# Performance work log

Measured on AMD Instinct MI355X. Metric: run time of the kernel, lower is better.

## Reference

```python
import jax, jax.numpy as jnp
import numpy as np

K = 16          # patch_size
P2 = 256        # patch_size**2
D_PD = 512      # learned base dictionary atoms (D_out_lam_pd)
D_LAM = 112     # adaptive atoms from sdict, = 8*14 (D_out_lam)
DD = D_PD + D_LAM  # 624
T = 5
INDICE = 112
MIN_V, MAX_V = 0.0, 1.0


def _idx(H, W, k, stride):
    oh = (H - k) // stride + 1
    ow = (W - k) // stride + 1
    r = jnp.arange(k)[:, None] + stride * jnp.arange(oh)[None, :]  # [k, oh]
    c = jnp.arange(k)[:, None] + stride * jnp.arange(ow)[None, :]  # [k, ow]
    return r[:, None, :, None], c[None, :, None, :], oh, ow


def _unfold(x, k, stride):
    # torch.nn.Unfold: [N, C*k*k, L] with (C, kh, kw) channel order, row-major L
    N, C, H, W = x.shape
    r, c, oh, ow = _idx(H, W, k, stride)
    return x[:, :, r, c].reshape(N, C * k * k, oh * ow)


def _fold(p, H, W, k):
    # torch.nn.functional.fold (col2im) with stride 1, overlap-add
    N, ckk, L = p.shape
    r, c, oh, ow = _idx(H, W, k, 1)
    C = ckk // (k * k)
    out = jnp.zeros((N, C, H, W), p.dtype)
    return out.at[:, :, r, c].add(p.reshape(N, C, k, k, oh, ow))


def _mlp(x, ws):
    # Linear + clamp(min=0) chain, no relu after last layer (dropout = eval identity)
    for w, b in ws[:-1]:
        x = jnp.maximum(x @ w + b, 0.0)
    w, b = ws[-1]
    return x @ w + b


def _cbam(x, w1, w2, conv_w):
    # standard CBAM: channel attention (shared MLP on avg+max pool) then 7x7 spatial attention
    def mlp(v):
        return jnp.maximum(v @ w1, 0.0) @ w2
    ca = jax.nn.sigmoid(mlp(x.mean(axis=(2, 3))) + mlp(x.max(axis=(2, 3))))
    x = x * ca[:, :, None, None]
    s = jnp.stack([x.mean(axis=1), x.max(axis=1)], axis=1)  # [N,2,h,w]
    sa = jax.lax.conv_general_dilated(s, conv_w, (1, 1), [(3, 3), (3, 3)],
                                      dimension_numbers=('NCHW', 'OIHW', 'NCHW'))
    return x * jax.nn.sigmoid(sa)


def _soft(x, l):
    return jnp.sign(x) * jnp.maximum(jnp.abs(x) - l, 0.0)


def _stage(img, Dict, c, sd_ws, ca1, ca2, saw, lam_ws, pd_ws, w_ws):
    N, C, H, W = img.shape
    uf = _unfold(img, K, 1).transpose(0, 2, 1)     # [N, L, 256]
    uf1 = _unfold(img, K, 8).transpose(0, 2, 1)    # [N, L1, 256]
    step = uf1.shape[1] // INDICE                  # static under jit
    ext = uf1[:, ::step, :][:, :INDICE, :]         # [N, 112, 256]
    sd = _mlp(ext, sd_ws)                          # linears1..4
    sd = sd / jnp.maximum(jnp.linalg.norm(sd, axis=-1, keepdims=True), 1e-12)
    sd = _cbam(sd.transpose(0, 2, 1).reshape(N, P2, 8, 14), ca1, ca2, saw)
    sd = sd.reshape(N, P2, INDICE)                 # [N, 256, 112]
    Dcat = jnp.concatenate([jnp.broadcast_to(Dict, (N,) + Dict.shape), sd], axis=-1)  # [N,256,624]
    # thresholds: l = cat(lpd, ls)
    thr = jnp.concatenate([_mlp(uf, pd_ws) / c, _mlp(uf, lam_ws) / c], axis=-1)  # [N,L,624]
    y = uf @ Dcat                                  # [N, L, 624]
    # S = (I - D^T D / c)^T; D^T D is symmetric so the transpose is a no-op
    S = jnp.eye(DD, dtype=img.dtype) - (Dcat.transpose(0, 2, 1) @ Dcat) / c
    z = _soft(y, thr)
    for _ in range(T):  # LISTA unrolled iterations (T static)
        z = _soft(z @ S + y / c, thr)
    Wg = jax.nn.sigmoid(_mlp(uf, w_ws))            # [N, L, 256]
    x_pred = jnp.clip(z @ Dcat.transpose(0, 2, 1), MIN_V, MAX_V) * Wg
    num = _fold(x_pred.transpose(0, 2, 1), H, W, K)
    den = _fold(Wg.transpose(0, 2, 1), H, W, K)    # fold of W * ones
    return num / den


def _forward(x, Dict, c, s1w, s1b, s2w, s2b, s3w, s3b, s4w, s4b, caw1, caw2, saw,
             a1w, a1b, a2w, a2b, a3w, a3b, p1w, p1b, p2w, p2b, p3w, p3b,
             b1w, b1b, b2w, b2b, b3w, b3b, q1w, q1b, q2w, q2b, q3w, q3b,
             w1w, w1b, w2w, w2b, w3w, w3b):
    sd_ws = [(s1w, s1b), (s2w, s2b), (s3w, s3b), (s4w, s4b)]
    w_ws = [(w1w, w1b), (w2w, w2b), (w3w, w3b)]
    res = _stage(x, Dict, c, sd_ws, caw1, caw2, saw,
                 [(a1w, a1b), (a2w, a2b), (a3w, a3b)],
                 [(p1w, p1b), (p2w, p2b), (p3w, p3b)], w_ws)
    res = _stage(res, Dict, c, sd_ws, caw1, caw2, saw,
                 [(b1w, b1b), (b2w, b2b), (b3w, b3b)],
                 [(q1w, q1b), (q2w, q2b), (q3w, q3b)], w_ws)
    return res


def setup_inputs() -> dict:
    key = jax.random.key(0)
    ks = iter(jax.random.split(key, 40))
    d = {}
    d['x'] = jax.random.uniform(next(ks), (2, 1, 128, 128), jnp.float32)
    Dm = jax.random.normal(next(ks), (P2, D_PD), jnp.float32)
    d['Dict'] = Dm / jnp.linalg.norm(Dm, axis=0, keepdims=True)  # unit-norm atoms
    d['c'] = jnp.asarray(10.0, jnp.float32)  # c > ||D^T D||_2
    dims = {'s1': (256, 512), 's2': (512, 1024), 's3': (1024, 512), 's4': (512, 256),
            'a1': (256, 1024), 'a2': (1024, 512), 'a3': (512, 112),
            'p1': (256, 1024), 'p2': (1024, 512), 'p3': (512, 512),
            'b1': (256, 1024), 'b2': (1024, 512), 'b3': (512, 112),
            'q1': (256, 1024), 'q2': (1024, 512), 'q3': (512, 512),
            'w1': (256, 1024), 'w2': (1024, 512), 'w3': (512, 256)}
    for name, (i, o) in dims.items():
        d[name + 'w'] = jax.random.normal(next(ks), (i, o), jnp.float32) / np.float32(np.sqrt(i))
        d[name + 'b'] = jnp.zeros((o,), jnp.float32)
    d['caw1'] = jax.random.normal(next(ks), (256, 512), jnp.float32) / np.float32(16.0)
    d['caw2'] = jax.random.normal(next(ks), (512, 256), jnp.float32) / np.float32(np.sqrt(512))
    d['saw'] = jax.random.normal(next(ks), (1, 2, 7, 7), jnp.float32) * np.float32(0.1)
    return d


def reference(x, Dict, c, s1w, s1b, s2w, s2b, s3w, s3b, s4w, s4b, caw1, caw2, saw,
              a1w, a1b, a2w, a2b, a3w, a3b, p1w, p1b, p2w, p2b, p3w, p3b,
              b1w, b1b, b2w, b2b, b3w, b3b, q1w, q1b, q2w, q2b, q3w, q3b,
              w1w, w1b, w2w, w2b, w3w, w3b):
    return _forward(x, Dict, c, s1w, s1b, s2w, s2b, s3w, s3b, s4w, s4b, caw1, caw2, saw,
                    a1w, a1b, a2w, a2b, a3w, a3b, p1w, p1b, p2w, p2b, p3w, p3b,
                    b1w, b1b, b2w, b2b, b3w, b3b, q1w, q1b, q2w, q2b, q3w, q3b,
                    w1w, w1b, w2w, w2b, w3w, w3b)
```

## Files before the change

### kernel.cpp

```cpp
#include <hip/hip_runtime.h>
#include <hip/hip_bf16.h>
#include <math.h>

#define L_LOC 12769
#define NB 2
#define NLR (NB * L_LOC)
#define NW 19

typedef short short8v __attribute__((ext_vector_type(8)));
typedef float f32x4 __attribute__((ext_vector_type(4)));
typedef __hip_bfloat16 bf16;

__device__ __forceinline__ float softf(float x, float l) {
  float a = fmaxf(fabsf(x) - l, 0.0f);
  return x > 0.0f ? a : (x < 0.0f ? -a : 0.0f);
}
__device__ __forceinline__ float sigf(float x) { return 1.0f / (1.0f + expf(-x)); }
__device__ __forceinline__ void split2(float v, bf16& h, bf16& l) {
  h = __float2bfloat16(v);
  l = __float2bfloat16(v - __bfloat162float(h));
}

enum { ME_RELU = 0, ME_SCALE = 1, ME_SIG = 2, ME_Y = 3, ME_SOFT = 4, ME_XP = 5,
       ME_SMAT = 6, ME_LIN = 7 };

template <int EPI, int TERMS, int WLO>
__global__ __launch_bounds__(256) void mgemm_k(
    const bf16* __restrict__ A, int lda, size_t aOff,
    const bf16* __restrict__ B0, const bf16* __restrict__ B1, int ldb, size_t bOff,
    void* __restrict__ Cv, int ldc, size_t cOff,
    bf16* __restrict__ Zp,
    const float* __restrict__ bias,
    const void* __restrict__ E1, const void* __restrict__ E2, int lde,
    const float* __restrict__ cptr, int bRow, int Rc, int r0, int N, int K)
{
  const int NPA = (TERMS >= 3) ? 2 : 1;
  const int NPB = (TERMS >= 2) ? 2 : 1;
  __shared__ char As[(TERMS >= 3) ? 2 : 1][8192];
  __shared__ char Bs[(TERMS >= 2) ? 2 : 1][8192];
  const int t = threadIdx.x;
  const int lane = t & 63, wv = t >> 6;
  const int wr = wv >> 1, wc = wv & 1;
  const int m0 = blockIdx.y * 128, n0 = blockIdx.x * 128;
  const int nb = (m0 >= bRow) ? 1 : 0;
  const bf16* __restrict__ Bt = nb ? B1 : B0;
  const int row16 = lane & 15, kg = lane >> 4;
  const int grow = t >> 2;
  const int gcol = (t & 3) * 8;
  f32x4 acc[4][4];
#pragma unroll
  for (int i = 0; i < 4; ++i)
#pragma unroll
    for (int j = 0; j < 4; ++j) { acc[i][j][0] = 0.f; acc[i][j][1] = 0.f; acc[i][j][2] = 0.f; acc[i][j][3] = 0.f; }

  for (int k0 = 0; k0 < K; k0 += 32) {
#pragma unroll
    for (int h = 0; h < NPA; ++h)
#pragma unroll
      for (int i = 0; i < 2; ++i) {
        const bf16* ga = A + h * aOff + (size_t)(m0 + i * 64 + grow) * lda + k0 + gcol;
        __builtin_amdgcn_global_load_lds(
            (const __attribute__((address_space(1))) void*)ga,
            (__attribute__((address_space(3))) void*)(As[h] + i * 4096 + wv * 1024), 16, 0, 0);
      }
#pragma unroll
    for (int h = 0; h < NPB; ++h)
#pragma unroll
      for (int i = 0; i < 2; ++i) {
        const bf16* gb = Bt + h * bOff + (size_t)(n0 + i * 64 + grow) * ldb + k0 + gcol;
        __builtin_amdgcn_global_load_lds(
            (const __attribute__((address_space(1))) void*)gb,
            (__attribute__((address_space(3))) void*)(Bs[h] + i * 4096 + wv * 1024), 16, 0, 0);
      }
    __syncthreads();
    short8v ah[4], al[4], bh[4], bl[4];
#pragma unroll
    for (int mi = 0; mi < 4; ++mi) {
      int o = (wr * 64 + mi * 16 + row16) * 64 + kg * 16;
      ah[mi] = *(const short8v*)(As[0] + o);
      if (TERMS >= 3) al[mi] = *(const short8v*)(As[NPA - 1] + o);
    }
#pragma unroll
    for (int ni = 0; ni < 4; ++ni) {
      int o = (wc * 64 + ni * 16 + row16) * 64 + kg * 16;
      bh[ni] = *(const short8v*)(Bs[0] + o);
      if (TERMS >= 2) bl[ni] = *(const short8v*)(Bs[NPB - 1] + o);
    }
#pragma unroll
    for (int mi = 0; mi < 4; ++mi)
#pragma unroll
      for (int ni = 0; ni < 4; ++ni) {
        if (TERMS >= 2)
          acc[mi][ni] = __builtin_amdgcn_mfma_f32_16x16x32_bf16(ah[mi], bl[ni], acc[mi][ni], 0, 0, 0);
        if (TERMS >= 3)
          acc[mi][ni] = __builtin_amdgcn_mfma_f32_16x16x32_bf16(al[mi], bh[ni], acc[mi][ni], 0, 0, 0);
        acc[mi][ni] = __builtin_amdgcn_mfma_f32_16x16x32_bf16(ah[mi], bh[ni], acc[mi][ni], 0, 0, 0);
      }
    __syncthreads();
  }

  float invc = 1.0f;
  if (EPI == ME_SCALE || EPI == ME_SOFT || EPI == ME_SMAT) invc = 1.0f / cptr[0];
  bf16* Cb = (bf16*)Cv;
  float* Cf = (float*)Cv;
  const bf16* E1b = (const bf16*)E1;
  const bf16* E2b = (const bf16*)E2;
  const float* E1f = (const float*)E1;
#pragma unroll
  for (int ni = 0; ni < 4; ++ni) {
    int col = n0 + wc * 64 + ni * 16 + row16;
    const bool colok = col < N;
    float bv = 0.0f;
    if ((EPI == ME_RELU || EPI == ME_SCALE || EPI == ME_SIG || EPI == ME_LIN) && colok)
      bv = bias[col];
#pragma unroll
    for (int mi = 0; mi < 4; ++mi) {
      int rowb = m0 + wr * 64 + mi * 16 + kg * 4;
#pragma unroll
      for (int r = 0; r < 4; ++r) {
        int row = rowb + r;
        float v = acc[mi][ni][r];
        if (EPI == ME_RELU) {
          if (colok) {
            float o = fmaxf(v + bv, 0.0f);
            size_t ci = (size_t)row * ldc + col;
            if (WLO) {
              bf16 h, l; split2(o, h, l);
              Cb[ci] = h; Cb[ci + cOff] = l;
            } else {
              Cb[ci] = __float2bfloat16(o);
            }
          }
        } else if (EPI == ME_LIN) {
          if (colok && row < Rc) Cf[(size_t)row * ldc + col] = v + bv;
        } else if (EPI == ME_SCALE) {
          if (colok) Cb[(size_t)row * ldc + col] = __float2bfloat16((v + bv) * invc);
        } else if (EPI == ME_SIG) {
          if (colok) {
            int rl = row - nb * bRow;
            if (rl < Rc && rl >= 0)
              Cf[(size_t)col * NLR + (size_t)nb * L_LOC + r0 + rl] = sigf(v + bv);
          }
        } else if (EPI == ME_Y) {
          if (colok) {
            size_t e = (size_t)row * lde + col;
            Cb[(size_t)row * ldc + col] = __float2bfloat16(v);
            float tv = __bfloat162float(E1b[e]);
            Zp[(size_t)row * 640 + col] = __float2bfloat16(softf(v, tv));
          }
        } else if (EPI == ME_SOFT) {
          if (colok) {
            size_t e = (size_t)row * lde + col;
            float yv = __bfloat162float(E1b[e]);
            float tv = __bfloat162float(E2b[e]);
            Cb[(size_t)row * ldc + col] = __float2bfloat16(softf(v + yv * invc, tv));
          }
        } else if (EPI == ME_XP) {
          int rl = row - nb * bRow;
          if (colok && rl < Rc && rl >= 0) {
            size_t g = (size_t)col * NLR + (size_t)nb * L_LOC + r0 + rl;
            Cf[g] = fminf(fmaxf(v, 0.0f), 1.0f) * E1f[g];
          }
        } else {
          float o = (row < 624 && col < 624) ? ((row == col ? 1.0f : 0.0f) - v * invc) : 0.0f;
          bf16 h, l; split2(o, h, l);
          size_t ci = (size_t)row * ldc + col;
          Cb[ci] = h; Cb[ci + cOff] = l;
        }
      }
    }
  }
}

static void mgemm(hipStream_t st, int EPI, int terms, int wlo,
                  const bf16* A, int lda, size_t aOff,
                  const bf16* B0, const bf16* B1, int ldb, size_t bOff,
                  void* C, int ldc, size_t cOff,
                  bf16* Zp,
                  const float* bias, const void* E1, const void* E2, int lde,
                  const float* cptr, int bRow, int Rc, int r0,
                  int Mp, int N, int K)
{
  dim3 grid((N + 127) / 128, Mp / 128), blk(256);
#define MG(ep, tm, wl) mgemm_k<ep, tm, wl><<<grid, blk, 0, st>>>(A, lda, aOff, B0, B1, ldb, bOff, C, ldc, cOff, Zp, bias, E1, E2, lde, cptr, bRow, Rc, r0, N, K)
  if (EPI == ME_RELU && terms == 1 && !wlo) { MG(ME_RELU, 1, 0); }
  else if (EPI == ME_RELU && terms == 1)    { MG(ME_RELU, 1, 1); }
  else if (EPI == ME_RELU)                  { MG(ME_RELU, 3, 1); }
  else if (EPI == ME_LIN)                   { MG(ME_LIN, 3, 0); }
  else if (EPI == ME_SCALE)                 { MG(ME_SCALE, 3, 0); }
  else if (EPI == ME_SIG)                   { MG(ME_SIG, 1, 0); }
  else if (EPI == ME_Y)                     { MG(ME_Y, 3, 0); }
  else if (EPI == ME_SOFT)                  { MG(ME_SOFT, 2, 0); }
  else if (EPI == ME_XP)                    { MG(ME_XP, 2, 0); }
  else                                      { MG(ME_SMAT, 3, 0); }
#undef MG
}

struct WTable {
  const float* src[NW];
  bf16* dst[NW];
  int K[NW], N[NW], Kp[NW], Np[NW];
  long long loOff[NW];
  int base[NW + 1];
};

__global__ void wtransall_k(WTable w) {
  int idx = blockIdx.x * 256 + threadIdx.x;
  if (idx >= w.base[NW]) return;
  int s = 0;
  while (s < NW - 1 && idx >= w.base[s + 1]) ++s;
  int li = idx - w.base[s];
  int Kp = w.Kp[s];
  int n = li / Kp, k = li - n * Kp;
  float v = (n < w.N[s] && k < w.K[s]) ? w.src[s][(size_t)k * w.N[s] + n] : 0.0f;
  bf16 h, l; split2(v, h, l);
  w.dst[s][li] = h;
  w.dst[s][li + w.loOff[s]] = l;
}

__global__ void extb_k(const float* __restrict__ img, bf16* __restrict__ dst) {
  int idx = blockIdx.x * 256 + threadIdx.x;
  int row = idx >> 8, p = idx & 255;
  float v = 0.0f;
  if (row < 224) {
    int n = row / 112, e = row - n * 112;
    int l1 = 2 * e, i1 = l1 / 15, j1 = l1 - i1 * 15;
    v = img[n * 16384 + (8 * i1 + (p >> 4)) * 128 + 8 * j1 + (p & 15)];
  }
  bf16 h, l; split2(v, h, l);
  dst[idx] = h; dst[idx + 65536] = l;
}

__global__ void rownorm224_k(float* sd) {
  int r = blockIdx.x, t = threadIdx.x;
  float v[4], s = 0.0f;
#pragma unroll
  for (int j = 0; j < 4; ++j) { v[j] = sd[r * 256 + t + 64 * j]; s += v[j] * v[j]; }
#pragma unroll
  for (int o = 1; o < 64; o <<= 1) s += __shfl_xor(s, o);
  float sc = 1.0f / fmaxf(sqrtf(s), 1e-12f);
#pragma unroll
  for (int j = 0; j < 4; ++j) sd[r * 256 + t + 64 * j] = v[j] * sc;
}

__global__ void meanmax_k(const float* __restrict__ sd, float* mv, float* xv) {
  int id = blockIdx.x * 256 + threadIdx.x;
  int n = id >> 8, ch = id & 255;
  float s = 0.0f, m = -INFINITY;
  for (int e = 0; e < 112; ++e) {
    float v = sd[(n * 112 + e) * 256 + ch];
    s += v; m = fmaxf(m, v);
  }
  mv[id] = s * (1.0f / 112.0f);
  xv[id] = m;
}

__global__ void cah_k(const float* __restrict__ mv, const float* __restrict__ xv,
                      const float* __restrict__ w1, float* hm, float* hx) {
  int id = blockIdx.x * 256 + threadIdx.x;
  int n = id >> 9, o = id & 511;
  float sm = 0.0f, sx = 0.0f;
#pragma unroll 4
  for (int i = 0; i < 256; ++i) {
    float w = w1[i * 512 + o];
    sm = fmaf(mv[n * 256 + i], w, sm);
    sx = fmaf(xv[n * 256 + i], w, sx);
  }
  hm[id] = fmaxf(sm, 0.0f);
  hx[id] = fmaxf(sx, 0.0f);
}

__global__ void cao_k(const float* __restrict__ hm, const float* __restrict__ hx,
                      const float* __restrict__ w2, float* ca) {
  int id = blockIdx.x * 256 + threadIdx.x;
  int n = id >> 8, ch = id & 255;
  float s = 0.0f;
#pragma unroll 4
  for (int o = 0; o < 512; ++o)
    s = fmaf(hm[n * 512 + o] + hx[n * 512 + o], w2[o * 256 + ch], s);
  ca[id] = sigf(s);
}

__global__ __launch_bounds__(256) void spatial_k(
    const float* __restrict__ sd, const float* __restrict__ ca,
    const float* __restrict__ saw, float* __restrict__ Dcat)
{
  __shared__ float smean[112], smax[112], sa[112];
  const int n = blockIdx.x;
  const int t = threadIdx.x, lane = t & 63, w = t >> 6;
  float cav[4];
#pragma unroll
  for (int c = 0; c < 4; ++c) cav[c] = ca[n * 256 + lane + 64 * c];
  for (int s = w * 28; s < w * 28 + 28; ++s) {
    float sum = 0.0f, mx = -INFINITY;
#pragma unroll
    for (int c = 0; c < 4; ++c) {
      int ch = lane + 64 * c;
      float v = sd[(n * 112 + s) * 256 + ch] * cav[c];
      Dcat[(size_t)n * 159744 + ch * 624 + 512 + s] = v;
      sum += v; mx = fmaxf(mx, v);
    }
#pragma unroll
    for (int o = 1; o < 64; o <<= 1) {
      sum += __shfl_xor(sum, o);
      mx = fmaxf(mx, __shfl_xor(mx, o));
    }
    if (lane == 0) { smean[s] = sum * (1.0f / 256.0f); smax[s] = mx; }
  }
  __syncthreads();
  if (t < 112) {
    int h = t / 14, wd = t % 14;
    float acc = 0.0f;
    for (int dh = 0; dh < 7; ++dh) {
      int hh = h + dh - 3; if (hh < 0 || hh >= 8) continue;
      for (int dw = 0; dw < 7; ++dw) {
        int ww = wd + dw - 3; if (ww < 0 || ww >= 14) continue;
        int sp = hh * 14 + ww;
        acc += smean[sp] * saw[dh * 7 + dw] + smax[sp] * saw[49 + dh * 7 + dw];
      }
    }
    sa[t] = sigf(acc);
  }
  __syncthreads();
  for (int s = w * 28; s < w * 28 + 28; ++s) {
    float sg = sa[s];
#pragma unroll
    for (int c = 0; c < 4; ++c) {
      int ch = lane + 64 * c;
      Dcat[(size_t)n * 159744 + ch * 624 + 512 + s] *= sg;
    }
  }
}

__global__ void dcatconv_k(const float* __restrict__ Dict, const float* __restrict__ Dc,
                           bf16* __restrict__ Db, bf16* __restrict__ DbT) {
  int idx = blockIdx.x * 256 + threadIdx.x;
  if (idx >= 327680) return;
  int n = idx / 163840, r = idx - n * 163840;
  int p = r / 640, a = r - p * 640;
  float v = 0.0f;
  if (a < 512)      v = Dict[p * 512 + a];
  else if (a < 624) v = Dc[(size_t)n * 159744 + p * 624 + a];
  bf16 h, l; split2(v, h, l);
  size_t base = (size_t)n * 327680;
  Db[base + p * 640 + a] = h;
  Db[base + 163840 + p * 640 + a] = l;
  DbT[base + (size_t)a * 256 + p] = h;
  DbT[base + 163840 + (size_t)a * 256 + p] = l;
}

__global__ void unfold_k(const float* __restrict__ img, bf16* __restrict__ uf,
                         int r0, int Rc, int bRowc, size_t pOff) {
  int bi = blockIdx.x;
  int nb = bi >= Rc;
  int rl = nb ? bi - Rc : bi;
  int row = nb * bRowc + rl;
  int p = threadIdx.x;
  int l = r0 + rl;
  int i0 = l / 113, j0 = l - i0 * 113;
  float v = img[nb * 16384 + (i0 + (p >> 4)) * 128 + j0 + (p & 15)];
  bf16 h, lo; split2(v, h, lo);
  size_t o = (size_t)row * 256 + p;
  uf[o] = h; uf[o + pOff] = lo;
}

__global__ void folddiv_k(const float* __restrict__ xpT, const float* __restrict__ wgT,
                          float* __restrict__ out) {
  int idx = blockIdx.x * 256 + threadIdx.x;
  if (idx >= 262144) return;
  int g = idx & 7;
  int pix = idx >> 3;
  int n = pix >> 14, rem = pix & 16383;
  int i = rem >> 7, j = rem & 127;
  float num = 0.0f, den = 0.0f;
  int kh0 = (i - 112 > 0) ? i - 112 : 0;
  int kh1 = (i < 15) ? i : 15;
  int kw0 = (j - 112 > 0) ? j - 112 : 0;
  int kw1 = (j < 15) ? j : 15;
  for (int kh = kh0 + ((g - kh0) & 7); kh <= kh1; kh += 8)
    for (int kw = kw0; kw <= kw1; ++kw) {
      int l = (i - kh) * 113 + (j - kw);
      size_t base = (size_t)(kh * 16 + kw) * NLR + (size_t)n * L_LOC + l;
      num += xpT[base];
      den += wgT[base];
    }
#pragma unroll
  for (int o = 1; o < 8; o <<= 1) {
    num += __shfl_xor(num, o);
    den += __shfl_xor(den, o);
  }
  if (g == 0) out[pix] = num / den;
}

struct Bufs {
  float *xp, *wg, *Dcat_f, *sd, *res;
  float *mv, *xv, *hm, *hx, *ca;
  bf16 *Db, *DbT, *Sb;
  bf16 *extb, *sdh1, *sdh2, *sdh3;
  bf16 *uf, *h1, *h2, *z, *zn, *thr, *y;
  size_t ufO, h2O;
  int R;
};

static void run_stage(hipStream_t st, const float* const* in, const float* img,
                      float* outimg, int pd0, int lam0,
                      bf16* const* WtPd, bf16* const* WtLam, bf16* const* WtW,
                      bf16* const* Ws, const Bufs& b)
{
  const float* cptr = in[2];
  const int BIG = 1 << 30;
  extb_k<<<dim3(256), dim3(256), 0, st>>>(img, b.extb);
  mgemm(st, ME_RELU, 3, 1, b.extb, 256, 65536, Ws[0], Ws[0], 256, 512 * 256,
        b.sdh1, 512, 256 * 512, 0, in[4], 0, 0, 0, cptr, BIG, 224, 0, 256, 512, 256);
  mgemm(st, ME_RELU, 3, 1, b.sdh1, 512, 256 * 512, Ws[1], Ws[1], 512, 1024 * 512,
        b.sdh2, 1024, 256 * 1024, 0, in[6], 0, 0, 0, cptr, BIG, 224, 0, 256, 1024, 512);
  mgemm(st, ME_RELU, 3, 1, b.sdh2, 1024, 256 * 1024, Ws[2], Ws[2], 1024, 512 * 1024,
        b.sdh3, 512, 256 * 512, 0, in[8], 0, 0, 0, cptr, BIG, 224, 0, 256, 512, 1024);
  mgemm(st, ME_LIN, 3, 0, b.sdh3, 512, 256 * 512, Ws[3], Ws[3], 512, 256 * 512,
        b.sd, 256, 0, 0, in[10], 0, 0, 0, cptr, BIG, 224, 0, 256, 256, 512);
  rownorm224_k<<<dim3(224), dim3(64), 0, st>>>(b.sd);
  meanmax_k<<<dim3(2), dim3(256), 0, st>>>(b.sd, b.mv, b.xv);
  cah_k<<<dim3(4), dim3(256), 0, st>>>(b.mv, b.xv, in[41], b.hm, b.hx);
  cao_k<<<dim3(2), dim3(256), 0, st>>>(b.hm, b.hx, in[42], b.ca);
  spatial_k<<<dim3(2), dim3(256), 0, st>>>(b.sd, b.ca, in[43], b.Dcat_f);
  dcatconv_k<<<dim3(1280), dim3(256), 0, st>>>(in[1], b.Dcat_f, b.Db, b.DbT);
  for (int n = 0; n < NB; ++n) {
    const bf16* Dt = b.DbT + (size_t)n * 327680;
    mgemm(st, ME_SMAT, 3, 0, Dt, 256, 163840, Dt, Dt, 256, 163840,
          b.Sb + (size_t)n * 819200, 640, 409600, 0,
          0, 0, 0, 0, cptr, BIG, 624, 0, 640, 640, 256);
  }

  for (int r0 = 0; r0 < L_LOC; r0 += b.R) {
    int Rc = L_LOC - r0; if (Rc > b.R) Rc = b.R;
    int bRowc = ((Rc + 127) / 128) * 128;
    int Mp = 2 * bRowc;
    unfold_k<<<dim3(2 * Rc), dim3(256), 0, st>>>(img, b.uf, r0, Rc, bRowc, b.ufO);
    mgemm(st, ME_RELU, 1, 0, b.uf, 256, b.ufO, WtPd[0], WtPd[0], 256, 1024 * 256,
          b.h1, 1024, 0, 0, in[pd0 + 1], 0, 0, 0, cptr, bRowc, Rc, r0, Mp, 1024, 256);
    mgemm(st, ME_RELU, 1, 1, b.h1, 1024, 0, WtPd[1], WtPd[1], 1024, 512 * 1024,
          b.h2, 512, b.h2O, 0, in[pd0 + 3], 0, 0, 0, cptr, bRowc, Rc, r0, Mp, 512, 1024);
    mgemm(st, ME_SCALE, 3, 0, b.h2, 512, b.h2O, WtPd[2], WtPd[2], 512, 512 * 512,
          b.thr, 640, 0, 0, in[pd0 + 5], 0, 0, 0, cptr, bRowc, Rc, r0, Mp, 512, 512);
    mgemm(st, ME_RELU, 1, 0, b.uf, 256, b.ufO, WtLam[0], WtLam[0], 256, 1024 * 256,
          b.h1, 1024, 0, 0, in[lam0 + 1], 0, 0, 0, cptr, bRowc, Rc, r0, Mp, 1024, 256);
    mgemm(st, ME_RELU, 1, 1, b.h1, 1024, 0, WtLam[1], WtLam[1], 1024, 512 * 1024,
          b.h2, 512, b.h2O, 0, in[lam0 + 3], 0, 0, 0, cptr, bRowc, Rc, r0, Mp, 512, 1024);
    mgemm(st, ME_SCALE, 3, 0, b.h2, 512, b.h2O, WtLam[2], WtLam[2], 512, 128 * 512,
          b.thr + 512, 640, 0, 0, in[lam0 + 5], 0, 0, 0, cptr, bRowc, Rc, r0, Mp, 112, 512);
    mgemm(st, ME_RELU, 1, 0, b.uf, 256, b.ufO, WtW[0], WtW[0], 256, 1024 * 256,
          b.h1, 1024, 0, 0, in[36], 0, 0, 0, cptr, bRowc, Rc, r0, Mp, 1024, 256);
    mgemm(st, ME_RELU, 1, 1, b.h1, 1024, 0, WtW[1], WtW[1], 1024, 512 * 1024,
          b.h2, 512, b.h2O, 0, in[38], 0, 0, 0, cptr, bRowc, Rc, r0, Mp, 512, 1024);
    mgemm(st, ME_SIG, 1, 0, b.h2, 512, b.h2O, WtW[2], WtW[2], 512, 256 * 512,
          b.wg, 0, 0, 0, in[40], 0, 0, 0, cptr, bRowc, Rc, r0, Mp, 256, 512);
    mgemm(st, ME_Y, 3, 0, b.uf, 256, b.ufO, b.DbT, b.DbT + 327680, 256, 163840,
          b.y, 640, 0, b.z, 0, b.thr, 0, 640, cptr, bRowc, Rc, r0, Mp, 624, 256);
    bf16* zi = b.z; bf16* zo = b.zn;
    for (int it = 0; it < 5; ++it) {
      mgemm(st, ME_SOFT, 2, 0, zi, 640, 0, b.Sb, b.Sb + 819200, 640, 409600,
            zo, 640, 0, 0, 0, b.y, b.thr, 640, cptr, bRowc, Rc, r0, Mp, 624, 640);
      bf16* tmp = zi; zi = zo; zo = tmp;
    }
    mgemm(st, ME_XP, 2, 0, zi, 640, 0, b.Db, b.Db + 327680, 640, 163840,
          b.xp, 0, 0, 0, 0, b.wg, 0, 0, cptr, bRowc, Rc, r0, Mp, 256, 640);
  }
  folddiv_k<<<dim3(1024), dim3(256), 0, st>>>(b.xp, b.wg, outimg);
}

extern "C" void kernel_launch(void* const* d_in, const int* in_sizes, int n_in,
                              void* d_out, int out_size, void* d_ws, size_t ws_size,
                              hipStream_t stream)
{
  (void)in_sizes; (void)n_in; (void)out_size;
  const float* const* in = (const float* const*)d_in;
  char* base = (char*)d_ws;
  size_t off = 0;
  auto allocf = [&](size_t nelem) -> float* {
    float* p = (float*)(base + off);
    off += ((nelem * 4 + 255) / 256) * 256;
    return p;
  };
  auto allocb2 = [&](size_t nelem) -> bf16* {
    bf16* p = (bf16*)(base + off);
    off += ((nelem * 2 * 2 + 255) / 256) * 256;
    return p;
  };
  auto allocb1 = [&](size_t nelem) -> bf16* {
    bf16* p = (bf16*)(base + off);
    off += ((nelem * 2 + 255) / 256) * 256;
    return p;
  };
  Bufs b;
  b.xp = allocf((size_t)NLR * 256);
  b.wg = allocf((size_t)NLR * 256);
  b.Dcat_f = allocf(2 * 256 * 624);
  b.sd = allocf(224 * 256);
  b.res = allocf(2 * 16384);
  b.mv = allocf(512); b.xv = allocf(512);
  b.hm = allocf(1024); b.hx = allocf(1024);
  b.ca = allocf(512);
  b.Db = allocb2(2 * 163840);
  b.DbT = allocb2(2 * 163840);
  b.Sb = allocb2(2 * 409600);
  b.extb = allocb2(256 * 256);
  b.sdh1 = allocb2(256 * 512);
  b.sdh2 = allocb2(256 * 1024);
  b.sdh3 = allocb2(256 * 512);

  bf16 *Wa[3], *Wp[3], *Wb[3], *Wq[3], *Ww[3], *Ws[4];
  WTable wt;
  int ne = 0, tot = 0;
  auto addw = [&](const float* src, bf16* dst, int K, int N, int Kp, int Np) {
    wt.src[ne] = src; wt.dst[ne] = dst;
    wt.K[ne] = K; wt.N[ne] = N; wt.Kp[ne] = Kp; wt.Np[ne] = Np;
    wt.loOff[ne] = (long long)Np * Kp; wt.base[ne] = tot;
    tot += Np * Kp; ++ne;
  };
  int sdK[4] = {256, 512, 1024, 512}, sdN[4] = {512, 1024, 512, 256}, sdIdx[4] = {3, 5, 7, 9};
  for (int i = 0; i < 4; ++i) {
    Ws[i] = allocb2((size_t)sdN[i] * sdK[i]);
    addw(in[sdIdx[i]], Ws[i], sdK[i], sdN[i], sdK[i], sdN[i]);
  }
  struct WD { bf16** slot; int idx, K, N, Kp, Np; };
  WD wd[15] = {
    {&Wa[0], 11, 256, 1024, 256, 1024}, {&Wa[1], 13, 1024, 512, 1024, 512}, {&Wa[2], 15, 512, 112, 512, 128},
    {&Wp[0], 17, 256, 1024, 256, 1024}, {&Wp[1], 19, 1024, 512, 1024, 512}, {&Wp[2], 21, 512, 512, 512, 512},
    {&Wb[0], 23, 256, 1024, 256, 1024}, {&Wb[1], 25, 1024, 512, 1024, 512}, {&Wb[2], 27, 512, 112, 512, 128},
    {&Wq[0], 29, 256, 1024, 256, 1024}, {&Wq[1], 31, 1024, 512, 1024, 512}, {&Wq[2], 33, 512, 512, 512, 512},
    {&Ww[0], 35, 256, 1024, 256, 1024}, {&Ww[1], 37, 1024, 512, 1024, 512}, {&Ww[2], 39, 512, 256, 512, 256},
  };
  for (int i = 0; i < 15; ++i) {
    *wd[i].slot = allocb2((size_t)wd[i].Np * wd[i].Kp);
    addw(in[wd[i].idx], *wd[i].slot, wd[i].K, wd[i].N, wd[i].Kp, wd[i].Np);
  }
  wt.base[NW] = tot;
  wtransall_k<<<dim3((tot + 255) / 256), dim3(256), 0, stream>>>(wt);

  long long avail = (long long)ws_size - (long long)off - (1 << 20);
  long long perrow2 = 2LL * (10240 + 64);
  int R = 12800;
  if (avail / perrow2 < 12800) R = (int)(avail / perrow2);
  R &= ~127;
  if (R < 128) R = 128;
  b.R = R;
  size_t rows2 = (size_t)2 * R;
  b.uf = allocb2(rows2 * 256);  b.ufO = rows2 * 256;
  b.h1 = allocb1(rows2 * 1024);
  b.h2 = allocb2(rows2 * 512);  b.h2O = rows2 * 512;
  b.z = allocb1(rows2 * 640);
  b.zn = allocb1(rows2 * 640);
  b.thr = allocb1(rows2 * 640);
  b.y = allocb1(rows2 * 640);

  run_stage(stream, in, in[0], b.res, 17, 11, Wp, Wa, Ww, Ws, b);
  run_stage(stream, in, b.res, (float*)d_out, 29, 23, Wq, Wb, Ww, Ws, b);
}
```

Measured before the change: 3.134 ms.

## Fuse five LISTA soft-threshold iterations into one kernel with z kept in LDS

Replaces the five separate ME_SOFT GEMM launches, each of which round-tripped z through global memory, with a single lista_k kernel. Each 64-row block keeps its z tile in swizzled shared memory across all iterations and streams the S matrix hi/lo parts from global memory. y and thr are now stored as fp32 instead of bf16, and the initial soft-threshold moves into the new kernel. The cost is that S is reread from global or L2 on every iteration, the workspace per row grows, and the wide per-wave accumulator arrays raise register pressure.

After: 6.586 ms. +110.2%, slower.

```diff
diff --git a/kernel.cpp b/kernel.cpp
--- a/kernel.cpp
+++ b/kernel.cpp
@@ -21,17 +21,15 @@
   l = __float2bfloat16(v - __bfloat162float(h));
 }
 
-enum { ME_RELU = 0, ME_SCALE = 1, ME_SIG = 2, ME_Y = 3, ME_SOFT = 4, ME_XP = 5,
-       ME_SMAT = 6, ME_LIN = 7 };
+enum { ME_RELU = 0, ME_SCALE = 1, ME_SIG = 2, ME_Y = 3, ME_XP = 5, ME_SMAT = 6, ME_LIN = 7 };
 
 template <int EPI, int TERMS, int WLO>
 __global__ __launch_bounds__(256) void mgemm_k(
     const bf16* __restrict__ A, int lda, size_t aOff,
     const bf16* __restrict__ B0, const bf16* __restrict__ B1, int ldb, size_t bOff,
     void* __restrict__ Cv, int ldc, size_t cOff,
-    bf16* __restrict__ Zp,
     const float* __restrict__ bias,
-    const void* __restrict__ E1, const void* __restrict__ E2, int lde,
+    const float* __restrict__ E1, int lde,
     const float* __restrict__ cptr, int bRow, int Rc, int r0, int N, int K)
 {
   const int NPA = (TERMS >= 3) ? 2 : 1;
@@ -100,12 +98,9 @@
   }
 
   float invc = 1.0f;
-  if (EPI == ME_SCALE || EPI == ME_SOFT || EPI == ME_SMAT) invc = 1.0f / cptr[0];
+  if (EPI == ME_SCALE || EPI == ME_SMAT) invc = 1.0f / cptr[0];
   bf16* Cb = (bf16*)Cv;
   float* Cf = (float*)Cv;
-  const bf16* E1b = (const bf16*)E1;
-  const bf16* E2b = (const bf16*)E2;
-  const float* E1f = (const float*)E1;
 #pragma unroll
   for (int ni = 0; ni < 4; ++ni) {
     int col = n0 + wc * 64 + ni * 16 + row16;
@@ -134,7 +129,7 @@
         } else if (EPI == ME_LIN) {
           if (colok && row < Rc) Cf[(size_t)row * ldc + col] = v + bv;
         } else if (EPI == ME_SCALE) {
-          if (colok) Cb[(size_t)row * ldc + col] = __float2bfloat16((v + bv) * invc);
+          if (colok) Cf[(size_t)row * ldc + col] = (v + bv) * invc;
         } else if (EPI == ME_SIG) {
           if (colok) {
             int rl = row - nb * bRow;
@@ -142,24 +137,12 @@
               Cf[(size_t)col * NLR + (size_t)nb * L_LOC + r0 + rl] = sigf(v + bv);
           }
         } else if (EPI == ME_Y) {
-          if (colok) {
-            size_t e = (size_t)row * lde + col;
-            Cb[(size_t)row * ldc + col] = __float2bfloat16(v);
-            float tv = __bfloat162float(E1b[e]);
-            Zp[(size_t)row * 640 + col] = __float2bfloat16(softf(v, tv));
-          }
-        } else if (EPI == ME_SOFT) {
-          if (colok) {
-            size_t e = (size_t)row * lde + col;
-            float yv = __bfloat162float(E1b[e]);
-            float tv = __bfloat162float(E2b[e]);
-            Cb[(size_t)row * ldc + col] = __float2bfloat16(softf(v + yv * invc, tv));
-          }
+          if (colok) Cf[(size_t)row * ldc + col] = v;
         } else if (EPI == ME_XP) {
           int rl = row - nb * bRow;
           if (colok && rl < Rc && rl >= 0) {
             size_t g = (size_t)col * NLR + (size_t)nb * L_LOC + r0 + rl;
-            Cf[g] = fminf(fmaxf(v, 0.0f), 1.0f) * E1f[g];
+            Cf[g] = fminf(fmaxf(v, 0.0f), 1.0f) * E1[g];
           }
         } else {
           float o = (row < 624 && col < 624) ? ((row == col ? 1.0f : 0.0f) - v * invc) : 0.0f;
@@ -176,13 +159,12 @@
                   const bf16* A, int lda, size_t aOff,
                   const bf16* B0, const bf16* B1, int ldb, size_t bOff,
                   void* C, int ldc, size_t cOff,
-                  bf16* Zp,
-                  const float* bias, const void* E1, const void* E2, int lde,
+                  const float* bias, const float* E1, int lde,
                   const float* cptr, int bRow, int Rc, int r0,
                   int Mp, int N, int K)
 {
   dim3 grid((N + 127) / 128, Mp / 128), blk(256);
-#define MG(ep, tm, wl) mgemm_k<ep, tm, wl><<<grid, blk, 0, st>>>(A, lda, aOff, B0, B1, ldb, bOff, C, ldc, cOff, Zp, bias, E1, E2, lde, cptr, bRow, Rc, r0, N, K)
+#define MG(ep, tm, wl) mgemm_k<ep, tm, wl><<<grid, blk, 0, st>>>(A, lda, aOff, B0, B1, ldb, bOff, C, ldc, cOff, bias, E1, lde, cptr, bRow, Rc, r0, N, K)
   if (EPI == ME_RELU && terms == 1 && !wlo) { MG(ME_RELU, 1, 0); }
   else if (EPI == ME_RELU && terms == 1)    { MG(ME_RELU, 1, 1); }
   else if (EPI == ME_RELU)                  { MG(ME_RELU, 3, 1); }
@@ -190,10 +172,100 @@
   else if (EPI == ME_SCALE)                 { MG(ME_SCALE, 3, 0); }
   else if (EPI == ME_SIG)                   { MG(ME_SIG, 1, 0); }
   else if (EPI == ME_Y)                     { MG(ME_Y, 3, 0); }
-  else if (EPI == ME_SOFT)                  { MG(ME_SOFT, 2, 0); }
   else if (EPI == ME_XP)                    { MG(ME_XP, 2, 0); }
   else                                      { MG(ME_SMAT, 3, 0); }
 #undef MG
+}
+
+__global__ __launch_bounds__(256, 2) void lista_k(
+    const float* __restrict__ y, const float* __restrict__ thr,
+    const bf16* __restrict__ S0, const bf16* __restrict__ S1,
+    bf16* __restrict__ zout, const float* __restrict__ cptr, int bRow)
+{
+  __shared__ bf16 zb[64 * 640];
+  const int t = threadIdx.x;
+  const int lane = t & 63, wv = t >> 6;
+  const int m0 = blockIdx.x * 64;
+  const bf16* __restrict__ S = (m0 >= bRow) ? S1 : S0;
+  const int row16 = lane & 15, kg = lane >> 4;
+  const float invc = 1.0f / cptr[0];
+  const int wbase = wv * 160;
+
+#pragma unroll
+  for (int ni = 0; ni < 10; ++ni) {
+    int col = wbase + ni * 16 + row16;
+    bool ok = col < 624;
+#pragma unroll
+    for (int mi = 0; mi < 4; ++mi)
+#pragma unroll
+      for (int r = 0; r < 4; ++r) {
+        int row = mi * 16 + kg * 4 + r;
+        float zv = 0.0f;
+        if (ok) {
+          size_t e = (size_t)(m0 + row) * 640 + col;
+          zv = softf(y[e], thr[e]);
+        }
+        int cb = (col * 2) ^ ((row & 7) << 4);
+        *(bf16*)((char*)zb + row * 1280 + cb) = __float2bfloat16(zv);
+      }
+  }
+  __syncthreads();
+
+  for (int it = 0; it < 5; ++it) {
+    f32x4 acc[4][10];
+#pragma unroll
+    for (int mi = 0; mi < 4; ++mi)
+#pragma unroll
+      for (int ni = 0; ni < 10; ++ni) {
+        acc[mi][ni][0] = 0.f; acc[mi][ni][1] = 0.f;
+        acc[mi][ni][2] = 0.f; acc[mi][ni][3] = 0.f;
+      }
+    for (int k0 = 0; k0 < 640; k0 += 32) {
+      short8v af[4];
+#pragma unroll
+      for (int mi = 0; mi < 4; ++mi) {
+        int row = mi * 16 + row16;
+        int cb = ((k0 + kg * 8) * 2) ^ ((row & 7) << 4);
+        af[mi] = *(const short8v*)((const char*)zb + row * 1280 + cb);
+      }
+#pragma unroll
+      for (int ni = 0; ni < 10; ++ni) {
+        const bf16* sp = S + (size_t)(wbase + ni * 16 + row16) * 640 + k0 + kg * 8;
+        short8v bh = *(const short8v*)sp;
+        short8v bl = *(const short8v*)(sp + 409600);
+#pragma unroll
+        for (int mi = 0; mi < 4; ++mi) {
+          acc[mi][ni] = __builtin_amdgcn_mfma_f32_16x16x32_bf16(af[mi], bl, acc[mi][ni], 0, 0, 0);
+          acc[mi][ni] = __builtin_amdgcn_mfma_f32_16x16x32_bf16(af[mi], bh, acc[mi][ni], 0, 0, 0);
+        }
+      }
+    }
+    __syncthreads();
+#pragma unroll
+    for (int ni = 0; ni < 10; ++ni) {
+      int col = wbase + ni * 16 + row16;
+      bool ok = col < 624;
+#pragma unroll
+      for (int mi = 0; mi < 4; ++mi)
+#pragma unroll
+        for (int r = 0; r < 4; ++r) {
+          int row = mi * 16 + kg * 4 + r;
+          float zv = 0.0f;
+          if (ok) {
+            size_t e = (size_t)(m0 + row) * 640 + col;
+            zv = softf(acc[mi][ni][r] + y[e] * invc, thr[e]);
+          }
+          int cb = (col * 2) ^ ((row & 7) << 4);
+          *(bf16*)((char*)zb + row * 1280 + cb) = __float2bfloat16(zv);
+        }
+    }
+    __syncthreads();
+  }
+  for (int i = t; i < 64 * 640; i += 256) {
+    int row = i / 640, col = i - row * 640;
+    int cb = (col * 2) ^ ((row & 7) << 4);
+    zout[(size_t)(m0 + row) * 640 + col] = *(const bf16*)((const char*)zb + row * 1280 + cb);
+  }
 }
 
 struct WTable {
@@ -397,7 +469,8 @@
   float *mv, *xv, *hm, *hx, *ca;
   bf16 *Db, *DbT, *Sb;
   bf16 *extb, *sdh1, *sdh2, *sdh3;
-  bf16 *uf, *h1, *h2, *z, *zn, *thr, *y;
+  bf16 *uf, *h1, *h2, *z;
+  float *thr, *y;
   size_t ufO, h2O;
   int R;
 };
@@ -411,13 +484,13 @@
   const int BIG = 1 << 30;
   extb_k<<<dim3(256), dim3(256), 0, st>>>(img, b.extb);
   mgemm(st, ME_RELU, 3, 1, b.extb, 256, 65536, Ws[0], Ws[0], 256, 512 * 256,
-        b.sdh1, 512, 256 * 512, 0, in[4], 0, 0, 0, cptr, BIG, 224, 0, 256, 512, 256);
+        b.sdh1, 512, 256 * 512, in[4], 0, 0, cptr, BIG, 224, 0, 256, 512, 256);
   mgemm(st, ME_RELU, 3, 1, b.sdh1, 512, 256 * 512, Ws[1], Ws[1], 512, 1024 * 512,
-        b.sdh2, 1024, 256 * 1024, 0, in[6], 0, 0, 0, cptr, BIG, 224, 0, 256, 1024, 512);
+        b.sdh2, 1024, 256 * 1024, in[6], 0, 0, cptr, BIG, 224, 0, 256, 1024, 512);
   mgemm(st, ME_RELU, 3, 1, b.sdh2, 1024, 256 * 1024, Ws[2], Ws[2], 1024, 512 * 1024,
-        b.sdh3, 512, 256 * 512, 0, in[8], 0, 0, 0, cptr, BIG, 224, 0, 256, 512, 1024);
+        b.sdh3, 512, 256 * 512, in[8], 0, 0, cptr, BIG, 224, 0, 256, 512, 1024);
   mgemm(st, ME_LIN, 3, 0, b.sdh3, 512, 256 * 512, Ws[3], Ws[3], 512, 256 * 512,
-        b.sd, 256, 0, 0, in[10], 0, 0, 0, cptr, BIG, 224, 0, 256, 256, 512);
+        b.sd, 256, 0, in[10], 0, 0, cptr, BIG, 224, 0, 256, 256, 512);
   rownorm224_k<<<dim3(224), dim3(64), 0, st>>>(b.sd);
   meanmax_k<<<dim3(2), dim3(256), 0, st>>>(b.sd, b.mv, b.xv);
   cah_k<<<dim3(4), dim3(256), 0, st>>>(b.mv, b.xv, in[41], b.hm, b.hx);
@@ -427,8 +500,8 @@
   for (int n = 0; n < NB; ++n) {
     const bf16* Dt = b.DbT + (size_t)n * 327680;
     mgemm(st, ME_SMAT, 3, 0, Dt, 256, 163840, Dt, Dt, 256, 163840,
-          b.Sb + (size_t)n * 819200, 640, 409600, 0,
-          0, 0, 0, 0, cptr, BIG, 624, 0, 640, 640, 256);
+          b.Sb + (size_t)n * 819200, 640, 409600,
+          0, 0, 0, cptr, BIG, 624, 0, 640, 640, 256);
   }
 
   for (int r0 = 0; r0 < L_LOC; r0 += b.R) {
@@ -437,33 +510,29 @@
     int Mp = 2 * bRowc;
     unfold_k<<<dim3(2 * Rc), dim3(256), 0, st>>>(img, b.uf, r0, Rc, bRowc, b.ufO);
     mgemm(st, ME_RELU, 1, 0, b.uf, 256, b.ufO, WtPd[0], WtPd[0], 256, 1024 * 256,
-          b.h1, 1024, 0, 0, in[pd0 + 1], 0, 0, 0, cptr, bRowc, Rc, r0, Mp, 1024, 256);
+          b.h1, 1024, 0, in[pd0 + 1], 0, 0, cptr, bRowc, Rc, r0, Mp, 1024, 256);
     mgemm(st, ME_RELU, 1, 1, b.h1, 1024, 0, WtPd[1], WtPd[1], 1024, 512 * 1024,
-          b.h2, 512, b.h2O, 0, in[pd0 + 3], 0, 0, 0, cptr, bRowc, Rc, r0, Mp, 512, 1024);
+          b.h2, 512, b.h2O, in[pd0 + 3], 0, 0, cptr, bRowc, Rc, r0, Mp, 512, 1024);
     mgemm(st, ME_SCALE, 3, 0, b.h2, 512, b.h2O, WtPd[2], WtPd[2], 512, 512 * 512,
-          b.thr, 640, 0, 0, in[pd0 + 5], 0, 0, 0, cptr, bRowc, Rc, r0, Mp, 512, 512);
+          b.thr, 640, 0, in[pd0 + 5], 0, 0, cptr, bRowc, Rc, r0, Mp, 512, 512);
     mgemm(st, ME_RELU, 1, 0, b.uf, 256, b.ufO, WtLam[0], WtLam[0], 256, 1024 * 256,
-          b.h1, 1024, 0, 0, in[lam0 + 1], 0, 0, 0, cptr, bRowc, Rc, r0, Mp, 1024, 256);
+          b.h1, 1024, 0, in[lam0 + 1], 0, 0, cptr, bRowc, Rc, r0, Mp, 1024, 256);
     mgemm(st, ME_RELU, 1, 1, b.h1, 1024, 0, WtLam[1], WtLam[1], 1024, 512 * 1024,
-          b.h2, 512, b.h2O, 0, in[lam0 + 3], 0, 0, 0, cptr, bRowc, Rc, r0, Mp, 512, 1024);
+          b.h2, 512, b.h2O, in[lam0 + 3], 0, 0, cptr, bRowc, Rc, r0, Mp, 512, 1024);
     mgemm(st, ME_SCALE, 3, 0, b.h2, 512, b.h2O, WtLam[2], WtLam[2], 512, 128 * 512,
-          b.thr + 512, 640, 0, 0, in[lam0 + 5], 0, 0, 0, cptr, bRowc, Rc, r0, Mp, 112, 512);
+          b.thr + 512, 640, 0, in[lam0 + 5], 0, 0, cptr, bRowc, Rc, r0, Mp, 112, 512);
     mgemm(st, ME_RELU, 1, 0, b.uf, 256, b.ufO, WtW[0], WtW[0], 256, 1024 * 256,
-          b.h1, 1024, 0, 0, in[36], 0, 0, 0, cptr, bRowc, Rc, r0, Mp, 1024, 256);
+          b.h1, 1024, 0, in[36], 0, 0, cptr, bRowc, Rc, r0, Mp, 1024, 256);
     mgemm(st, ME_RELU, 1, 1, b.h1, 1024, 0, WtW[1], WtW[1], 1024, 512 * 1024,
-          b.h2, 512, b.h2O, 0, in[38], 0, 0, 0, cptr, bRowc, Rc, r0, Mp, 512, 1024);
+          b.h2, 512, b.h2O, in[38], 0, 0, cptr, bRowc, Rc, r0, Mp, 512, 1024);
     mgemm(st, ME_SIG, 1, 0, b.h2, 512, b.h2O, WtW[2], WtW[2], 512, 256 * 512,
-          b.wg, 0, 0, 0, in[40], 0, 0, 0, cptr, bRowc, Rc, r0, Mp, 256, 512);
+          b.wg, 0, 0, in[40], 0, 0, cptr, bRowc, Rc, r0, Mp, 256, 512);
     mgemm(st, ME_Y, 3, 0, b.uf, 256, b.ufO, b.DbT, b.DbT + 327680, 256, 163840,
-          b.y, 640, 0, b.z, 0, b.thr, 0, 640, cptr, bRowc, Rc, r0, Mp, 624, 256);
-    bf16* zi = b.z; bf16* zo = b.zn;
-    for (int it = 0; it < 5; ++it) {
-      mgemm(st, ME_SOFT, 2, 0, zi, 640, 0, b.Sb, b.Sb + 819200, 640, 409600,
-            zo, 640, 0, 0, 0, b.y, b.thr, 640, cptr, bRowc, Rc, r0, Mp, 624, 640);
-      bf16* tmp = zi; zi = zo; zo = tmp;
-    }
-    mgemm(st, ME_XP, 2, 0, zi, 640, 0, b.Db, b.Db + 327680, 640, 163840,
-          b.xp, 0, 0, 0, 0, b.wg, 0, 0, cptr, bRowc, Rc, r0, Mp, 256, 640);
+          b.y, 640, 0, 0, 0, 0, cptr, bRowc, Rc, r0, Mp, 624, 256);
+    lista_k<<<dim3(Mp / 64), dim3(256), 0, st>>>(
+        b.y, b.thr, b.Sb, b.Sb + 819200 * 1, b.z, cptr, bRowc);
+    mgemm(st, ME_XP, 2, 0, b.z, 640, 0, b.Db, b.Db + 327680, 640, 163840,
+          b.xp, 0, 0, 0, b.wg, 0, cptr, bRowc, Rc, r0, Mp, 256, 640);
   }
   folddiv_k<<<dim3(1024), dim3(256), 0, st>>>(b.xp, b.wg, outimg);
 }
@@ -538,7 +607,7 @@
   wtransall_k<<<dim3((tot + 255) / 256), dim3(256), 0, stream>>>(wt);
 
   long long avail = (long long)ws_size - (long long)off - (1 << 20);
-  long long perrow2 = 2LL * (10240 + 64);
+  long long perrow2 = 2LL * (11520 + 64);
   int R = 12800;
   if (avail / perrow2 < 12800) R = (int)(avail / perrow2);
   R &= ~127;
@@ -549,9 +618,8 @@
   b.h1 = allocb1(rows2 * 1024);
   b.h2 = allocb2(rows2 * 512);  b.h2O = rows2 * 512;
   b.z = allocb1(rows2 * 640);
-  b.zn = allocb1(rows2 * 640);
-  b.thr = allocb1(rows2 * 640);
-  b.y = allocb1(rows2 * 640);
+  b.thr = allocf(rows2 * 640);
+  b.y = allocf(rows2 * 640);
 
   run_stage(stream, in, in[0], b.res, 17, 11, Wp, Wa, Ww, Ws, b);
   run_stage(stream, in, b.res, (float*)d_out, 29, 23, Wq, Wb, Ww, Ws, b);
```
